# Kernel optimization log

Measured on AMD Instinct MI355X. Metric: run time of the kernel, lower is better.

## Reference

```python
import jax, jax.numpy as jnp
import numpy as np

PAD = 0
NEG_INF = -1e30

B, P, Q, D = 32, 4096, 64, 128  # batch, passage len, question len, nhid


def setup_inputs() -> dict:
    key = jax.random.key(0)
    k1, k2, k3, k4, k5, k6 = jax.random.split(key, 6)
    return {
        "tensor_H": jax.random.normal(k1, (B, P, D), dtype=jnp.float32),
        "tensor_U": jax.random.normal(k2, (B, Q, D), dtype=jnp.float32),
        "M": jax.random.normal(k3, (B, P, D), dtype=jnp.float32),
        "sentence_word_rep": jax.random.randint(k4, (B, P), 0, 10000, dtype=jnp.int64),
        "W_attn": jax.random.normal(k5, (D, D), dtype=jnp.float32) / np.sqrt(D),
        "W_cls": jax.random.normal(k6, (5 * D, 2), dtype=jnp.float32) / np.sqrt(5 * D),
    }


def reference(tensor_H, tensor_U, M, sentence_word_rep, W_attn, W_cls):
    # Matrix attention (bilinear): S[b,p,q] = h_p^T W u_q  -> (B, P, Q)
    S = jnp.einsum("bpd,de,bqe->bpq", tensor_H, W_attn, tensor_U)
    # context-to-query: softmax over question axis, then bmm with U
    c2q = jnp.einsum("bpq,bqd->bpd", jax.nn.softmax(S, axis=2), tensor_U)
    # query-to-context: softmax over passage axis of row-max, weighted sum of H
    b_attn = jax.nn.softmax(jnp.max(S, axis=2), axis=-1)        # (B, P)
    q2c = jnp.einsum("bp,bpd->bd", b_attn, tensor_H)[:, None, :]  # (B, 1, D) broadcast over P
    # G = [H; c2q; H*c2q; H*q2c] -> (B, P, 4D); G_M = [G; M] -> (B, P, 5D)
    G_M = jnp.concatenate(
        [tensor_H, c2q, tensor_H * c2q, tensor_H * q2c, M], axis=2
    )
    # masked max-pool over passage positions (mask where token == PAD)
    pad_mask = (sentence_word_rep == PAD)[:, :, None]           # (B, P, 1)
    pooled = jnp.max(jnp.where(pad_mask, NEG_INF, G_M), axis=1)  # (B, 5D)
    # final linear classifier (no bias)
    return pooled @ W_cls                                        # (B, 2)
```

## Files before the change

### kernel.cpp

```cpp
#include <hip/hip_runtime.h>

#define B_ 32
#define P_ 4096
#define Q_ 64
#define D_ 128

#define T_SIZE (B_*Q_*D_)
#define PART_STRIDE 772
#define NCHUNK 32
#define CHUNK_ROWS 128

typedef __attribute__((ext_vector_type(8))) short bf16x8;
typedef __attribute__((ext_vector_type(4))) float f32x4;

__device__ __forceinline__ unsigned int asu(float x) { return __float_as_uint(x); }
__device__ __forceinline__ float asf(unsigned int x) { return __uint_as_float(x); }

__global__ __launch_bounds__(256) void k_T(const float* __restrict__ U,
                                           const float* __restrict__ W,
                                           float* __restrict__ T) {
  __shared__ float Wl[128*132];
  __shared__ float Ul[8*128];
  const int b = blockIdx.x >> 3, qc = blockIdx.x & 7;
  const int t = threadIdx.x;
#pragma unroll
  for (int k = 0; k < 16; ++k) {
    int i = t*4 + k*1024;
    float4 wv = *(const float4*)(W + i);
    int d = i >> 7, e = i & 127;
    *(float4*)(&Wl[d*132 + e]) = wv;
  }
  {
    int i = t*4;
    int q = i >> 7, e = i & 127;
    *(float4*)(&Ul[q*128 + e]) =
        *(const float4*)(U + ((size_t)(b*Q_ + qc*8 + q))*D_ + e);
  }
  __syncthreads();
  const int d = t & 127, qhalf = t >> 7;
#pragma unroll
  for (int pass = 0; pass < 4; ++pass) {
    const int q = pass*2 + qhalf;
    float acc = 0.f;
#pragma unroll
    for (int e = 0; e < 128; e += 4) {
      float4 wv = *(float4*)(&Wl[d*132 + e]);
      float4 uv = *(float4*)(&Ul[q*128 + e]);
      acc += wv.x*uv.x + wv.y*uv.y + wv.z*uv.z + wv.w*uv.w;
    }
    T[((size_t)(b*Q_ + qc*8 + q))*D_ + d] = acc;
  }
}

__global__ __launch_bounds__(512, 4) void k_main(
    const float* __restrict__ H, const float* __restrict__ U,
    const float* __restrict__ M, const int* __restrict__ tok,
    const float* __restrict__ T, float* __restrict__ part) {
  __shared__ __align__(16) char smem[16384*4 + 1536];
  char* Thi = smem;
  char* Tlo = smem + 16384;
  char* Utl = smem + 32768;
  char* Pl  = smem + 49152;
  float* mrow  = (float*)(smem + 65536);
  float* rzrow = (float*)(smem + 66048);
  int*   tkl   = (int*)(smem + 66560);

  const int bid = blockIdx.x;
  const int b = bid >> 5, chunk = bid & 31;
  const int t = threadIdx.x, wv = t >> 6, l = t & 63;
  const int r15 = l & 15, g4 = l >> 4;

  const float* Tb = T + (size_t)b*Q_*D_;
  const float* Ub = U + (size_t)b*Q_*D_;
#pragma unroll
  for (int k = 0; k < 4; ++k) {
    int i = t*4 + k*2048;
    int q = i >> 7, d = i & 127;
    float4 tv = *(const float4*)(Tb + i);
    unsigned int b0 = asu(tv.x), b1 = asu(tv.y), b2 = asu(tv.z), b3 = asu(tv.w);
    unsigned int hi0 = (b1 & 0xFFFF0000u) | (b0 >> 16);
    unsigned int hi1 = (b3 & 0xFFFF0000u) | (b2 >> 16);
    float l0 = tv.x - asf(b0 & 0xFFFF0000u);
    float l1 = tv.y - asf(b1 & 0xFFFF0000u);
    float l2 = tv.z - asf(b2 & 0xFFFF0000u);
    float l3 = tv.w - asf(b3 & 0xFFFF0000u);
    unsigned int lo0 = (asu(l1) & 0xFFFF0000u) | (asu(l0) >> 16);
    unsigned int lo1 = (asu(l3) & 0xFFFF0000u) | (asu(l2) >> 16);
    int ta = (q*256 + 2*d) ^ ((q & 7) << 4);
    *(uint2*)(Thi + ta) = make_uint2(hi0, hi1);
    *(uint2*)(Tlo + ta) = make_uint2(lo0, lo1);
    float4 uv = *(const float4*)(Ub + i);
    float uvv[4] = {uv.x, uv.y, uv.z, uv.w};
#pragma unroll
    for (int j = 0; j < 4; ++j) {
      int dd = d + j;
      int ua = (dd*128 + 2*q) ^ ((dd & 7) << 4);
      *(unsigned short*)(Utl + ua) = (unsigned short)(asu(uvv[j]) >> 16);
    }
  }
  if (t < 128) tkl[t] = tok[b*P_ + chunk*CHUNK_ROWS + t];
  __syncthreads();

  const int rowB = b*P_ + chunk*CHUNK_ROWS;

  {
    const int lrow0 = wv*16;
    f32x4 sacc[4];
#pragma unroll
    for (int qt = 0; qt < 4; ++qt) sacc[qt] = (f32x4){0.f, 0.f, 0.f, 0.f};
    const float* Arow = H + (size_t)(rowB + lrow0 + r15)*D_;
#pragma unroll
    for (int ks = 0; ks < 4; ++ks) {
      const float* ap = Arow + ks*32 + g4*8;
      float4 fa = *(const float4*)(ap);
      float4 fb = *(const float4*)(ap + 4);
      union { bf16x8 v; unsigned int u[4]; } Ah, Al;
      {
        unsigned int a0 = asu(fa.x), a1 = asu(fa.y), a2 = asu(fa.z), a3 = asu(fa.w);
        unsigned int c0 = asu(fb.x), c1 = asu(fb.y), c2 = asu(fb.z), c3 = asu(fb.w);
        Ah.u[0] = (a1 & 0xFFFF0000u) | (a0 >> 16);
        Ah.u[1] = (a3 & 0xFFFF0000u) | (a2 >> 16);
        Ah.u[2] = (c1 & 0xFFFF0000u) | (c0 >> 16);
        Ah.u[3] = (c3 & 0xFFFF0000u) | (c2 >> 16);
        float p0 = fa.x - asf(a0 & 0xFFFF0000u);
        float p1 = fa.y - asf(a1 & 0xFFFF0000u);
        float p2 = fa.z - asf(a2 & 0xFFFF0000u);
        float p3 = fa.w - asf(a3 & 0xFFFF0000u);
        float p4 = fb.x - asf(c0 & 0xFFFF0000u);
        float p5 = fb.y - asf(c1 & 0xFFFF0000u);
        float p6 = fb.z - asf(c2 & 0xFFFF0000u);
        float p7 = fb.w - asf(c3 & 0xFFFF0000u);
        Al.u[0] = (asu(p1) & 0xFFFF0000u) | (asu(p0) >> 16);
        Al.u[1] = (asu(p3) & 0xFFFF0000u) | (asu(p2) >> 16);
        Al.u[2] = (asu(p5) & 0xFFFF0000u) | (asu(p4) >> 16);
        Al.u[3] = (asu(p7) & 0xFFFF0000u) | (asu(p6) >> 16);
      }
#pragma unroll
      for (int qt = 0; qt < 4; ++qt) {
        int q = qt*16 + r15;
        int off = (q*256 + ks*64 + g4*16) ^ ((q & 7) << 4);
        bf16x8 bh = *(bf16x8*)(Thi + off);
        bf16x8 bl = *(bf16x8*)(Tlo + off);
        sacc[qt] = __builtin_amdgcn_mfma_f32_16x16x32_bf16(Al.v, bh, sacc[qt], 0, 0, 0);
        sacc[qt] = __builtin_amdgcn_mfma_f32_16x16x32_bf16(Ah.v, bl, sacc[qt], 0, 0, 0);
        sacc[qt] = __builtin_amdgcn_mfma_f32_16x16x32_bf16(Ah.v, bh, sacc[qt], 0, 0, 0);
      }
    }
    float m[4];
#pragma unroll
    for (int j = 0; j < 4; ++j)
      m[j] = fmaxf(fmaxf(sacc[0][j], sacc[1][j]), fmaxf(sacc[2][j], sacc[3][j]));
#pragma unroll
    for (int off = 1; off <= 8; off <<= 1)
#pragma unroll
      for (int j = 0; j < 4; ++j) m[j] = fmaxf(m[j], __shfl_xor(m[j], off));
    float Zp[4] = {0.f, 0.f, 0.f, 0.f};
#pragma unroll
    for (int qt = 0; qt < 4; ++qt)
#pragma unroll
      for (int j = 0; j < 4; ++j) {
        float e = __expf(sacc[qt][j] - m[j]);
        Zp[j] += e;
        int p = lrow0 + g4*4 + j, q = qt*16 + r15;
        int off = (p*128 + 2*q) ^ ((p & 7) << 4);
        *(unsigned short*)(Pl + off) = (unsigned short)(asu(e) >> 16);
      }
#pragma unroll
    for (int off = 1; off <= 8; off <<= 1)
#pragma unroll
      for (int j = 0; j < 4; ++j) Zp[j] += __shfl_xor(Zp[j], off);
    if (r15 == 0) {
#pragma unroll
      for (int j = 0; j < 4; ++j) {
        mrow[lrow0 + g4*4 + j]  = m[j];
        rzrow[lrow0 + g4*4 + j] = __builtin_amdgcn_rcpf(Zp[j]);
      }
    }
  }
  __syncthreads();

  float m0 = mrow[l], m1 = mrow[l + 64];
  float Lm = fmaxf(m0, m1);
#pragma unroll
  for (int off = 1; off <= 32; off <<= 1) Lm = fmaxf(Lm, __shfl_xor(Lm, off));
  float ssum = __expf(m0 - Lm) + __expf(m1 - Lm);
#pragma unroll
  for (int off = 1; off <= 32; off <<= 1) ssum += __shfl_xor(ssum, off);

  const int dd = wv*16 + r15;
  bf16x8 bu0 = *(bf16x8*)(Utl + ((dd*128 +  0 + g4*16) ^ ((dd & 7) << 4)));
  bf16x8 bu1 = *(bf16x8*)(Utl + ((dd*128 + 64 + g4*16) ^ ((dd & 7) << 4)));

  float v = 0.f, xH = -3.0e38f, nH = 3.0e38f;
  float xC = -3.0e38f, xHC = -3.0e38f, xM = -3.0e38f;
#pragma unroll
  for (int rti = 0; rti < 8; ++rti) {
    const int rt = (rti + wv) & 7;
    f32x4 pv = (f32x4){0.f, 0.f, 0.f, 0.f};
    {
      int pr0 = rt*16 + r15;
      bf16x8 a0 = *(bf16x8*)(Pl + ((pr0*128 +  0 + g4*16) ^ ((r15 & 7) << 4)));
      bf16x8 a1 = *(bf16x8*)(Pl + ((pr0*128 + 64 + g4*16) ^ ((r15 & 7) << 4)));
      pv = __builtin_amdgcn_mfma_f32_16x16x32_bf16(a0, bu0, pv, 0, 0, 0);
      pv = __builtin_amdgcn_mfma_f32_16x16x32_bf16(a1, bu1, pv, 0, 0, 0);
    }
    const float* Hrow = H + (size_t)(rowB + rt*16 + g4*4)*D_ + dd;
    const float* Mrow = M + (size_t)(rowB + rt*16 + g4*4)*D_ + dd;
#pragma unroll
    for (int j = 0; j < 4; ++j) {
      const int row = rt*16 + g4*4 + j;
      const int tkv = tkl[row];
      const float bmax = tkv ? 0.f : -1.0e38f;
      const float bmin = tkv ? 0.f : 1.0e38f;
      float pr = __expf(mrow[row] - Lm);
      float h  = Hrow[(size_t)j*D_];
      float mv = Mrow[(size_t)j*D_];
      float c  = pv[j] * rzrow[row];
      v   += pr*h;
      xH   = fmaxf(xH,  h + bmax);
      nH   = fminf(nH,  h + bmin);
      xC   = fmaxf(xC,  c + bmax);
      xHC  = fmaxf(xHC, h*c + bmax);
      xM   = fmaxf(xM,  mv + bmax);
    }
  }
#pragma unroll
  for (int off = 16; off <= 32; off <<= 1) {
    v   += __shfl_xor(v, off);
    xH   = fmaxf(xH,  __shfl_xor(xH,  off));
    nH   = fminf(nH,  __shfl_xor(nH,  off));
    xC   = fmaxf(xC,  __shfl_xor(xC,  off));
    xHC  = fmaxf(xHC, __shfl_xor(xHC, off));
    xM   = fmaxf(xM,  __shfl_xor(xM,  off));
  }
  float* pp = part + (size_t)bid*PART_STRIDE;
  if (t == 0) { pp[0] = Lm; pp[1] = ssum; }
  if (g4 == 0) {
    pp[2 + dd]   = v;
    pp[130 + dd] = xH;
    pp[258 + dd] = nH;
    pp[386 + dd] = xC;
    pp[514 + dd] = xHC;
    pp[642 + dd] = xM;
  }
}

__global__ __launch_bounds__(128) void k_final(const float* __restrict__ part,
                                               const float* __restrict__ Wc,
                                               float* __restrict__ out) {
  __shared__ float pooled[640];
  __shared__ float r0s[2], r1s[2];
  const int b = blockIdx.x, t = threadIdx.x;
  const float* pb = part + (size_t)b*NCHUNK*PART_STRIDE;
  float L = -3.0e38f;
#pragma unroll
  for (int c = 0; c < NCHUNK; ++c) L = fmaxf(L, pb[c*PART_STRIDE]);
  float S = 0.f, V = 0.f;
  float mh = -3.0e38f, nh = 3.0e38f, mc = -3.0e38f, mhc = -3.0e38f, mm = -3.0e38f;
#pragma unroll
  for (int c = 0; c < NCHUNK; ++c) {
    const float* p = pb + c*PART_STRIDE;
    float e = __expf(p[0] - L);
    S += p[1]*e;
    V += p[2 + t]*e;
    mh  = fmaxf(mh,  p[130 + t]);
    nh  = fminf(nh,  p[258 + t]);
    mc  = fmaxf(mc,  p[386 + t]);
    mhc = fmaxf(mhc, p[514 + t]);
    mm  = fmaxf(mm,  p[642 + t]);
  }
  float q2c = V / S;
  pooled[t]       = mh;
  pooled[128 + t] = mc;
  pooled[256 + t] = mhc;
  pooled[384 + t] = (q2c >= 0.f) ? q2c*mh : q2c*nh;
  pooled[512 + t] = mm;
  __syncthreads();
  float a0 = 0.f, a1 = 0.f;
#pragma unroll
  for (int k = t; k < 640; k += 128) {
    float pv = pooled[k];
    a0 += pv*Wc[k*2 + 0];
    a1 += pv*Wc[k*2 + 1];
  }
#pragma unroll
  for (int off = 32; off; off >>= 1) {
    a0 += __shfl_xor(a0, off);
    a1 += __shfl_xor(a1, off);
  }
  if ((t & 63) == 0) { r0s[t >> 6] = a0; r1s[t >> 6] = a1; }
  __syncthreads();
  if (t == 0) {
    out[b*2 + 0] = r0s[0] + r0s[1];
    out[b*2 + 1] = r1s[0] + r1s[1];
  }
}

extern "C" void kernel_launch(void* const* d_in, const int* in_sizes, int n_in,
                              void* d_out, int out_size, void* d_ws, size_t ws_size,
                              hipStream_t stream) {
  const float* H   = (const float*)d_in[0];
  const float* U   = (const float*)d_in[1];
  const float* M   = (const float*)d_in[2];
  const int*   tok = (const int*)d_in[3];
  const float* Wa  = (const float*)d_in[4];
  const float* Wc  = (const float*)d_in[5];
  float* out = (float*)d_out;
  float* wsf = (float*)d_ws;
  float* T    = wsf;
  float* part = wsf + T_SIZE;

  hipLaunchKernelGGL(k_T,     dim3(256),        dim3(256), 0, stream, U, Wa, T);
  hipLaunchKernelGGL(k_main,  dim3(B_*NCHUNK),  dim3(512), 0, stream, H, U, M, tok, T, part);
  hipLaunchKernelGGL(k_final, dim3(B_),         dim3(128), 0, stream, part, Wc, out);
}
```

Before: 58.27 us.

## Pre-split T into bf16 hi/lo swizzled global buffers in k_T, drop LDS staging

```diff
diff --git a/kernel.cpp b/kernel.cpp
--- a/kernel.cpp
+++ b/kernel.cpp
@@ -5,10 +5,10 @@
 #define Q_ 64
 #define D_ 128
 
-#define T_SIZE (B_*Q_*D_)
 #define PART_STRIDE 772
 #define NCHUNK 32
 #define CHUNK_ROWS 128
+#define TWS_BYTES (96*16384)
 
 typedef __attribute__((ext_vector_type(8))) short bf16x8;
 typedef __attribute__((ext_vector_type(4))) float f32x4;
@@ -18,7 +18,7 @@
 
 __global__ __launch_bounds__(256) void k_T(const float* __restrict__ U,
                                            const float* __restrict__ W,
-                                           float* __restrict__ T) {
+                                           char* __restrict__ Tws) {
   __shared__ float Wl[128*132];
   __shared__ float Ul[8*128];
   const int b = blockIdx.x >> 3, qc = blockIdx.x & 7;
@@ -38,68 +38,52 @@
   }
   __syncthreads();
   const int d = t & 127, qhalf = t >> 7;
+  char* Thi = Tws + b*16384;
+  char* Tlo = Tws + 32*16384 + b*16384;
+  char* Utl = Tws + 64*16384 + b*16384;
 #pragma unroll
   for (int pass = 0; pass < 4; ++pass) {
-    const int q = pass*2 + qhalf;
+    const int ql = pass*2 + qhalf;
+    const int qg = qc*8 + ql;
     float acc = 0.f;
 #pragma unroll
     for (int e = 0; e < 128; e += 4) {
       float4 wv = *(float4*)(&Wl[d*132 + e]);
-      float4 uv = *(float4*)(&Ul[q*128 + e]);
+      float4 uv = *(float4*)(&Ul[ql*128 + e]);
       acc += wv.x*uv.x + wv.y*uv.y + wv.z*uv.z + wv.w*uv.w;
     }
-    T[((size_t)(b*Q_ + qc*8 + q))*D_ + d] = acc;
+    unsigned int au = asu(acc);
+    unsigned short hs = (unsigned short)(au >> 16);
+    float lo = acc - asf(au & 0xFFFF0000u);
+    unsigned short ls = (unsigned short)(asu(lo) >> 16);
+    int ta = (qg*256 + 2*d) ^ ((qg & 7) << 4);
+    *(unsigned short*)(Thi + ta) = hs;
+    *(unsigned short*)(Tlo + ta) = ls;
+    float uval = Ul[ql*128 + d];
+    int ua = (d*128 + 2*qg) ^ ((d & 7) << 4);
+    *(unsigned short*)(Utl + ua) = (unsigned short)(asu(uval) >> 16);
   }
 }
 
-__global__ __launch_bounds__(512, 4) void k_main(
-    const float* __restrict__ H, const float* __restrict__ U,
-    const float* __restrict__ M, const int* __restrict__ tok,
-    const float* __restrict__ T, float* __restrict__ part) {
-  __shared__ __align__(16) char smem[16384*4 + 1536];
-  char* Thi = smem;
-  char* Tlo = smem + 16384;
-  char* Utl = smem + 32768;
-  char* Pl  = smem + 49152;
-  float* mrow  = (float*)(smem + 65536);
-  float* rzrow = (float*)(smem + 66048);
-  int*   tkl   = (int*)(smem + 66560);
+__global__ __launch_bounds__(512, 8) void k_main(
+    const float* __restrict__ H, const float* __restrict__ M,
+    const int* __restrict__ tok, const char* __restrict__ Tws,
+    float* __restrict__ part) {
+  __shared__ __align__(16) char Pl[16384];
+  __shared__ float mrow[128];
+  __shared__ float rzrow[128];
+  __shared__ float prow[128];
+  __shared__ int   tkl[128];
 
   const int bid = blockIdx.x;
   const int b = bid >> 5, chunk = bid & 31;
   const int t = threadIdx.x, wv = t >> 6, l = t & 63;
   const int r15 = l & 15, g4 = l >> 4;
-
-  const float* Tb = T + (size_t)b*Q_*D_;
-  const float* Ub = U + (size_t)b*Q_*D_;
-#pragma unroll
-  for (int k = 0; k < 4; ++k) {
-    int i = t*4 + k*2048;
-    int q = i >> 7, d = i & 127;
-    float4 tv = *(const float4*)(Tb + i);
-    unsigned int b0 = asu(tv.x), b1 = asu(tv.y), b2 = asu(tv.z), b3 = asu(tv.w);
-    unsigned int hi0 = (b1 & 0xFFFF0000u) | (b0 >> 16);
-    unsigned int hi1 = (b3 & 0xFFFF0000u) | (b2 >> 16);
-    float l0 = tv.x - asf(b0 & 0xFFFF0000u);
-    float l1 = tv.y - asf(b1 & 0xFFFF0000u);
-    float l2 = tv.z - asf(b2 & 0xFFFF0000u);
-    float l3 = tv.w - asf(b3 & 0xFFFF0000u);
-    unsigned int lo0 = (asu(l1) & 0xFFFF0000u) | (asu(l0) >> 16);
-    unsigned int lo1 = (asu(l3) & 0xFFFF0000u) | (asu(l2) >> 16);
-    int ta = (q*256 + 2*d) ^ ((q & 7) << 4);
-    *(uint2*)(Thi + ta) = make_uint2(hi0, hi1);
-    *(uint2*)(Tlo + ta) = make_uint2(lo0, lo1);
-    float4 uv = *(const float4*)(Ub + i);
-    float uvv[4] = {uv.x, uv.y, uv.z, uv.w};
-#pragma unroll
-    for (int j = 0; j < 4; ++j) {
-      int dd = d + j;
-      int ua = (dd*128 + 2*q) ^ ((dd & 7) << 4);
-      *(unsigned short*)(Utl + ua) = (unsigned short)(asu(uvv[j]) >> 16);
-    }
-  }
+  const char* Thi = Tws + b*16384;
+  const char* Tlo = Tws + 32*16384 + b*16384;
+  const char* Utl = Tws + 64*16384 + b*16384;
+
   if (t < 128) tkl[t] = tok[b*P_ + chunk*CHUNK_ROWS + t];
-  __syncthreads();
 
   const int rowB = b*P_ + chunk*CHUNK_ROWS;
 
@@ -139,8 +123,8 @@
       for (int qt = 0; qt < 4; ++qt) {
         int q = qt*16 + r15;
         int off = (q*256 + ks*64 + g4*16) ^ ((q & 7) << 4);
-        bf16x8 bh = *(bf16x8*)(Thi + off);
-        bf16x8 bl = *(bf16x8*)(Tlo + off);
+        bf16x8 bh = *(const bf16x8*)(Thi + off);
+        bf16x8 bl = *(const bf16x8*)(Tlo + off);
         sacc[qt] = __builtin_amdgcn_mfma_f32_16x16x32_bf16(Al.v, bh, sacc[qt], 0, 0, 0);
         sacc[qt] = __builtin_amdgcn_mfma_f32_16x16x32_bf16(Ah.v, bl, sacc[qt], 0, 0, 0);
         sacc[qt] = __builtin_amdgcn_mfma_f32_16x16x32_bf16(Ah.v, bh, sacc[qt], 0, 0, 0);
@@ -186,10 +170,12 @@
   float ssum = __expf(m0 - Lm) + __expf(m1 - Lm);
 #pragma unroll
   for (int off = 1; off <= 32; off <<= 1) ssum += __shfl_xor(ssum, off);
+  if (t < 128) prow[t] = __expf(mrow[t] - Lm);
+  __syncthreads();
 
   const int dd = wv*16 + r15;
-  bf16x8 bu0 = *(bf16x8*)(Utl + ((dd*128 +  0 + g4*16) ^ ((dd & 7) << 4)));
-  bf16x8 bu1 = *(bf16x8*)(Utl + ((dd*128 + 64 + g4*16) ^ ((dd & 7) << 4)));
+  bf16x8 bu0 = *(const bf16x8*)(Utl + ((dd*128 +  0 + g4*16) ^ ((dd & 7) << 4)));
+  bf16x8 bu1 = *(const bf16x8*)(Utl + ((dd*128 + 64 + g4*16) ^ ((dd & 7) << 4)));
 
   float v = 0.f, xH = -3.0e38f, nH = 3.0e38f;
   float xC = -3.0e38f, xHC = -3.0e38f, xM = -3.0e38f;
@@ -212,7 +198,7 @@
       const int tkv = tkl[row];
       const float bmax = tkv ? 0.f : -1.0e38f;
       const float bmin = tkv ? 0.f : 1.0e38f;
-      float pr = __expf(mrow[row] - Lm);
+      float pr = prow[row];
       float h  = Hrow[(size_t)j*D_];
       float mv = Mrow[(size_t)j*D_];
       float c  = pv[j] * rzrow[row];
@@ -306,11 +292,11 @@
   const float* Wa  = (const float*)d_in[4];
   const float* Wc  = (const float*)d_in[5];
   float* out = (float*)d_out;
-  float* wsf = (float*)d_ws;
-  float* T    = wsf;
-  float* part = wsf + T_SIZE;
-
-  hipLaunchKernelGGL(k_T,     dim3(256),        dim3(256), 0, stream, U, Wa, T);
-  hipLaunchKernelGGL(k_main,  dim3(B_*NCHUNK),  dim3(512), 0, stream, H, U, M, tok, T, part);
+  char* wsc = (char*)d_ws;
+  char* Tws = wsc;
+  float* part = (float*)(wsc + TWS_BYTES);
+
+  hipLaunchKernelGGL(k_T,     dim3(256),        dim3(256), 0, stream, U, Wa, Tws);
+  hipLaunchKernelGGL(k_main,  dim3(B_*NCHUNK),  dim3(512), 0, stream, H, M, tok, Tws, part);
   hipLaunchKernelGGL(k_final, dim3(B_),         dim3(128), 0, stream, part, Wc, out);
 }
```

New measurement: 65.10 us. 11.7% more time.
